# Performance work log

Measured on AMD Instinct MI355X. Metric: run time of the kernel, lower is better.

## Reference

```python
import jax, jax.numpy as jnp
import numpy as np

N_NODES = 100000
N_EDGES = 1280000
IN_DIM = 64
HID = 64
OUT_DIM = 2
N_GRAPHS = 1000
BN_EPS = 1e-5


def setup_inputs() -> dict:
    key = jax.random.key(0)
    ks = jax.random.split(key, 16)
    x = jax.random.normal(ks[0], (N_NODES, IN_DIM), dtype=jnp.float32)
    edge_index = jax.random.randint(ks[1], (2, N_EDGES), 0, N_NODES, dtype=jnp.int64)
    batch = jnp.sort(jax.random.randint(ks[2], (N_NODES,), 0, N_GRAPHS, dtype=jnp.int64))
    # He-init linear weights (stored as [in, out] so forward is x @ W)
    def he(k, fan_in, fan_out):
        return jax.random.normal(k, (fan_in, fan_out), dtype=jnp.float32) * np.sqrt(2.0 / fan_in)
    return {
        "x": x,
        "edge_index": edge_index,
        "batch": batch,
        "bn_in_g": jnp.ones((IN_DIM,), jnp.float32),
        "bn_in_b": jnp.zeros((IN_DIM,), jnp.float32),
        "W1": he(ks[3], IN_DIM, HID), "b1": jnp.zeros((HID,), jnp.float32),
        "g1": jnp.ones((HID,), jnp.float32), "be1": jnp.zeros((HID,), jnp.float32),
        "W2": he(ks[4], HID, HID), "b2": jnp.zeros((HID,), jnp.float32),
        "g2": jnp.ones((HID,), jnp.float32), "be2": jnp.zeros((HID,), jnp.float32),
        "Wout": he(ks[5], HID, OUT_DIM), "bout": jnp.zeros((OUT_DIM,), jnp.float32),
    }


def _batchnorm(x, g, b):
    # training-mode BN over the node dimension (biased variance, as torch uses for normalization)
    m = jnp.mean(x, axis=0)
    v = jnp.mean(jnp.square(x - m), axis=0)
    return (x - m) * jax.lax.rsqrt(v + BN_EPS) * g + b


def _gcn_norm(edge_index, n):
    # PyG GCNConv normalization with added self-loops:
    # norm_e = deg[src]^-1/2 * deg[dst]^-1/2, deg computed on A + I over targets.
    row = jnp.concatenate([edge_index[0], jnp.arange(n, dtype=edge_index.dtype)])
    col = jnp.concatenate([edge_index[1], jnp.arange(n, dtype=edge_index.dtype)])
    deg = jax.ops.segment_sum(jnp.ones_like(col, dtype=jnp.float32), col, num_segments=n)
    dinv = jnp.where(deg > 0, jax.lax.rsqrt(deg), 0.0)
    norm = dinv[row] * dinv[col]
    return row, col, norm


def _gcn_conv(x, W, b, row, col, norm, n):
    h = x @ W                                   # [N, out]
    msg = h[row] * norm[:, None]                # gather over edges (incl. self-loops)
    agg = jax.ops.segment_sum(msg, col, num_segments=n)
    return agg + b


def reference(x, edge_index, batch, bn_in_g, bn_in_b, W1, b1, g1, be1, W2, b2, g2, be2, Wout, bout):
    n = x.shape[0]
    row, col, norm = _gcn_norm(edge_index, n)
    h = _batchnorm(x, bn_in_g, bn_in_b)         # input BN (dropout = identity in eval)
    h = _gcn_conv(h, W1, b1, row, col, norm, n)
    h = _batchnorm(jax.nn.relu(h), g1, be1)
    h = _gcn_conv(h, W2, b2, row, col, norm, n)
    h = _batchnorm(jax.nn.relu(h), g2, be2)
    # global mean pool per graph
    sums = jax.ops.segment_sum(h, batch, num_segments=N_GRAPHS)
    cnts = jax.ops.segment_sum(jnp.ones((n,), h.dtype), batch, num_segments=N_GRAPHS)
    pooled = sums / jnp.maximum(cnts, 1.0)[:, None]
    return pooled @ Wout + bout                 # [N_GRAPHS, OUT_DIM]
```

## Files before the change

kernel.cpp:

```cpp
#include <hip/hip_runtime.h>
#include <math.h>

#define N_NODES 100000
#define N_EDGES 1280000
#define DIM 64
#define N_GRAPHS 1000
#define BN_EPS 1e-5f
#define NB 392
#define P1B 256
#define P1E 5000
#define SB 400
#define WIN 128
#define NWIN (N_EDGES / WIN)
#define GU 8
#define NSLOT 32

__device__ __forceinline__ unsigned int bf16_rtn2(float a, float b) {
    unsigned int ua = __float_as_uint(a);
    unsigned int ub = __float_as_uint(b);
    ua = (ua + 0x7FFFu + ((ua >> 16) & 1u)) >> 16;
    ub = (ub + 0x7FFFu + ((ub >> 16) & 1u)) >> 16;
    return ua | (ub << 16);
}
__device__ __forceinline__ unsigned short bf16r(float a) {
    unsigned int u = __float_as_uint(a);
    return (unsigned short)((u + 0x7FFFu + ((u >> 16) & 1u)) >> 16);
}
__device__ __forceinline__ float bfup(unsigned short u) {
    return __uint_as_float(((unsigned int)u) << 16);
}

__global__ __launch_bounds__(256) void k_p1hist(const int* __restrict__ ei,
                                                const int* __restrict__ batch,
                                                const float* __restrict__ X,
                                                int* __restrict__ bh,
                                                int* __restrict__ start,
                                                float* __restrict__ gsum,
                                                float* __restrict__ gsumsq) {
    int t = threadIdx.x;
    if (blockIdx.x < P1B) {
        __shared__ int hist[NB];
        for (int b = t; b < NB; b += 256) hist[b] = 0;
        __syncthreads();
        int e0 = blockIdx.x * P1E;
        #pragma unroll 4
        for (int e = e0 + t; e < e0 + P1E; e += 256)
            atomicAdd(&hist[ei[N_EDGES + e] >> 8], 1);
        __syncthreads();
        for (int b = t; b < NB; b += 256) bh[b * P1B + blockIdx.x] = hist[b];
    } else if (blockIdx.x < P1B + SB) {
        int grp = blockIdx.x - P1B;
        int j = t & 63, rg = t >> 6;
        int base = grp * 250;
        float s = 0.f, s2 = 0.f;
        for (int i = base + rg; i < base + 250; i += 4) {
            float v = X[i * DIM + j];
            s += v; s2 += v * v;
        }
        __shared__ float ls[256], ls2[256];
        ls[t] = s; ls2[t] = s2;
        __syncthreads();
        if (t < 64) {
            int slot = (grp & (NSLOT - 1)) * DIM;
            s  = ls[j]  + ls[64 + j]  + ls[128 + j]  + ls[192 + j];
            s2 = ls2[j] + ls2[64 + j] + ls2[128 + j] + ls2[192 + j];
            atomicAdd(&gsum[slot + j], s);
            atomicAdd(&gsumsq[slot + j], s2);
        }
    } else {
        int i = (blockIdx.x - P1B - SB) * 256 + t;
        if (i < N_NODES) {
            int cur = batch[i];
            if (i == 0) { for (int q = 0; q <= cur; q++) start[q] = 0; }
            else {
                int prev = batch[i - 1];
                for (int q = prev + 1; q <= cur; q++) start[q] = i;
            }
            if (i == N_NODES - 1)
                for (int q = cur + 1; q <= N_GRAPHS; q++) start[q] = N_NODES;
        }
    }
}

__global__ void k_scan1(const int* __restrict__ bh, int* __restrict__ iscan,
                        int* __restrict__ bsum) {
    __shared__ int ls[256];
    int i = blockIdx.x * 256 + threadIdx.x;
    int v = bh[i];
    ls[threadIdx.x] = v;
    __syncthreads();
    for (int off = 1; off < 256; off <<= 1) {
        int tv = (threadIdx.x >= off) ? ls[threadIdx.x - off] : 0;
        __syncthreads();
        ls[threadIdx.x] += tv;
        __syncthreads();
    }
    iscan[i] = ls[threadIdx.x];
    if (threadIdx.x == 255) bsum[blockIdx.x] = ls[255];
}

__global__ void k_scan2(const int* __restrict__ bsum, int* __restrict__ boff) {
    __shared__ int ls[512];
    int t = threadIdx.x;
    int v0 = (t < NB) ? bsum[t] : 0;
    ls[t] = v0;
    __syncthreads();
    for (int off = 1; off < 512; off <<= 1) {
        int v = (t >= off) ? ls[t - off] : 0;
        __syncthreads();
        ls[t] += v;
        __syncthreads();
    }
    if (t < NB) boff[t] = ls[t] - v0;
}

__global__ __launch_bounds__(256) void k_p1scat(const int* __restrict__ ei,
                                                const int* __restrict__ bh,
                                                const int* __restrict__ iscan,
                                                const int* __restrict__ boff,
                                                int2* __restrict__ tmp) {
    __shared__ int cur[NB];
    int blk = blockIdx.x;
    for (int b = threadIdx.x; b < NB; b += 256) {
        int i = b * P1B + blk;
        cur[b] = boff[b] + iscan[i] - bh[i];
    }
    __syncthreads();
    int e0 = blk * P1E;
    for (int e = e0 + threadIdx.x; e < e0 + P1E; e += 256) {
        int r = ei[e], c = ei[N_EDGES + e];
        int pos = atomicAdd(&cur[c >> 8], 1);
        tmp[pos] = make_int2(r, c);
    }
}

__global__ __launch_bounds__(256) void k_p2a(const int2* __restrict__ tmp,
                                             const int* __restrict__ bh,
                                             const int* __restrict__ iscan,
                                             const int* __restrict__ boff,
                                             int* __restrict__ rowstart,
                                             float* __restrict__ dinv,
                                             int* __restrict__ winnode) {
    int b = blockIdx.x, t = threadIdx.x;
    int bstart = boff[b] + iscan[b * 256] - bh[b * 256];
    int bend = (b == NB - 1) ? N_EDGES
                             : (boff[b + 1] + iscan[(b + 1) * 256] - bh[(b + 1) * 256]);
    __shared__ int cnt[256], scn[256];
    cnt[t] = 0;
    __syncthreads();
    for (int e = bstart + t; e < bend; e += 256)
        atomicAdd(&cnt[tmp[e].y & 255], 1);
    __syncthreads();
    scn[t] = cnt[t];
    __syncthreads();
    for (int off = 1; off < 256; off <<= 1) {
        int v = (t >= off) ? scn[t - off] : 0;
        __syncthreads();
        scn[t] += v;
        __syncthreads();
    }
    int node = b * 256 + t;
    int rs = bstart + scn[t] - cnt[t];
    if (node <= N_NODES) rowstart[node] = rs;
    if (node < N_NODES) {
        int deg = cnt[t];
        dinv[node] = 1.0f / sqrtf((float)(deg + 1));
        int re = rs + deg;
        for (int w = (rs + WIN - 1) / WIN; w * WIN < re; ++w) winnode[w] = node;
    }
}

__global__ __launch_bounds__(256) void k_p2b(const int2* __restrict__ tmp,
                                             const int* __restrict__ bh,
                                             const int* __restrict__ iscan,
                                             const int* __restrict__ boff,
                                             const int* __restrict__ rowstart,
                                             int* __restrict__ csr) {
    int b = blockIdx.x, t = threadIdx.x;
    int bstart = boff[b] + iscan[b * 256] - bh[b * 256];
    int bend = (b == NB - 1) ? N_EDGES
                             : (boff[b + 1] + iscan[(b + 1) * 256] - bh[(b + 1) * 256]);
    __shared__ int curs[256];
    int node = b * 256 + t;
    curs[t] = (node < N_NODES) ? rowstart[node] : 0;
    __syncthreads();
    for (int e = bstart + t; e < bend; e += 256) {
        int2 rec = tmp[e];
        int pos = atomicAdd(&curs[rec.y & 255], 1);
        csr[pos] = rec.x;
    }
}

__global__ void k_bnfold(float* __restrict__ gsum, float* __restrict__ gsumsq,
                         const float* __restrict__ g, const float* __restrict__ b,
                         const float* __restrict__ W,
                         float* __restrict__ scale, float* __restrict__ cshift) {
    int j = threadIdx.x;
    float ms = 0.f, m2 = 0.f;
    for (int k = 0; k < NSLOT; k++) {
        ms += gsum[k * DIM + j];   gsum[k * DIM + j] = 0.f;
        m2 += gsumsq[k * DIM + j]; gsumsq[k * DIM + j] = 0.f;
    }
    float mean = ms * (1.0f / N_NODES);
    float var  = m2 * (1.0f / N_NODES) - mean * mean;
    float inv  = 1.0f / sqrtf(var + BN_EPS);
    float sc   = g[j] * inv;
    scale[j] = sc;
    __shared__ float shl[64];
    shl[j] = b[j] - mean * sc;
    __syncthreads();
    float s = 0.f;
    for (int k = 0; k < DIM; k++) s += shl[k] * W[k * DIM + j];
    cshift[j] = s;
}

__global__ void k_bnfinal(const float* __restrict__ gsum, const float* __restrict__ gsumsq,
                          const float* __restrict__ g, const float* __restrict__ b,
                          float* __restrict__ scale, float* __restrict__ shift) {
    int j = threadIdx.x;
    float ms = 0.f, m2 = 0.f;
    for (int k = 0; k < NSLOT; k++) { ms += gsum[k * DIM + j]; m2 += gsumsq[k * DIM + j]; }
    float mean = ms * (1.0f / N_NODES);
    float var  = m2 * (1.0f / N_NODES) - mean * mean;
    float inv  = 1.0f / sqrtf(var + BN_EPS);
    float sc   = g[j] * inv;
    scale[j] = sc;
    shift[j] = b[j] - mean * sc;
}

__global__ __launch_bounds__(256) void k_gemm_f32(const float* __restrict__ X,
                                                  const float* __restrict__ W,
                                                  const float* __restrict__ scale,
                                                  const float* __restrict__ cshift,
                                                  const float* __restrict__ dinv,
                                                  unsigned short* __restrict__ T) {
    __shared__ float Wl[64 * 64];
    __shared__ float Al[64 * 65];
    for (int t = threadIdx.x; t < 4096; t += 256) Wl[t] = W[t] * scale[t >> 6];
    int row0 = blockIdx.x * 64;
    for (int t = threadIdx.x; t < 4096; t += 256) {
        int r = t >> 6, k = t & 63;
        int i = row0 + r;
        Al[r * 65 + k] = (i < N_NODES) ? X[(size_t)i * DIM + k] : 0.f;
    }
    __syncthreads();
    int r = threadIdx.x & 63;
    int q = threadIdx.x >> 6;
    float acc[16];
    #pragma unroll
    for (int jj = 0; jj < 16; jj++) acc[jj] = cshift[q * 16 + jj];
    #pragma unroll 4
    for (int k = 0; k < 64; k++) {
        float a = Al[r * 65 + k];
        const float4* wv = (const float4*)&Wl[k * 64 + q * 16];
        float4 w0 = wv[0], w1 = wv[1], w2 = wv[2], w3 = wv[3];
        acc[0]  += a * w0.x; acc[1]  += a * w0.y; acc[2]  += a * w0.z; acc[3]  += a * w0.w;
        acc[4]  += a * w1.x; acc[5]  += a * w1.y; acc[6]  += a * w1.z; acc[7]  += a * w1.w;
        acc[8]  += a * w2.x; acc[9]  += a * w2.y; acc[10] += a * w2.z; acc[11] += a * w2.w;
        acc[12] += a * w3.x; acc[13] += a * w3.y; acc[14] += a * w3.z; acc[15] += a * w3.w;
    }
    int i = row0 + r;
    if (i < N_NODES) {
        float dv = dinv[i];
        unsigned int pk[8];
        #pragma unroll
        for (int jj = 0; jj < 8; jj++)
            pk[jj] = bf16_rtn2(acc[2 * jj] * dv, acc[2 * jj + 1] * dv);
        uint4* outv = (uint4*)&T[(size_t)i * DIM + q * 16];
        outv[0] = make_uint4(pk[0], pk[1], pk[2], pk[3]);
        outv[1] = make_uint4(pk[4], pk[5], pk[6], pk[7]);
    }
}

__global__ __launch_bounds__(256) void k_gemm_b16(const unsigned short* __restrict__ X,
                                                  const float* __restrict__ W,
                                                  const float* __restrict__ scale,
                                                  const float* __restrict__ cshift,
                                                  const float* __restrict__ dinv,
                                                  unsigned short* __restrict__ T) {
    __shared__ float Wl[64 * 64];
    __shared__ float Al[64 * 65];
    for (int t = threadIdx.x; t < 4096; t += 256) Wl[t] = W[t] * scale[t >> 6];
    int row0 = blockIdx.x * 64;
    for (int t = threadIdx.x; t < 4096; t += 256) {
        int r = t >> 6, k = t & 63;
        int i = row0 + r;
        Al[r * 65 + k] = (i < N_NODES) ? bfup(X[(size_t)i * DIM + k]) : 0.f;
    }
    __syncthreads();
    int r = threadIdx.x & 63;
    int q = threadIdx.x >> 6;
    float acc[16];
    #pragma unroll
    for (int jj = 0; jj < 16; jj++) acc[jj] = cshift[q * 16 + jj];
    #pragma unroll 4
    for (int k = 0; k < 64; k++) {
        float a = Al[r * 65 + k];
        const float4* wv = (const float4*)&Wl[k * 64 + q * 16];
        float4 w0 = wv[0], w1 = wv[1], w2 = wv[2], w3 = wv[3];
        acc[0]  += a * w0.x; acc[1]  += a * w0.y; acc[2]  += a * w0.z; acc[3]  += a * w0.w;
        acc[4]  += a * w1.x; acc[5]  += a * w1.y; acc[6]  += a * w1.z; acc[7]  += a * w1.w;
        acc[8]  += a * w2.x; acc[9]  += a * w2.y; acc[10] += a * w2.z; acc[11] += a * w2.w;
        acc[12] += a * w3.x; acc[13] += a * w3.y; acc[14] += a * w3.z; acc[15] += a * w3.w;
    }
    int i = row0 + r;
    if (i < N_NODES) {
        float dv = dinv[i];
        unsigned int pk[8];
        #pragma unroll
        for (int jj = 0; jj < 8; jj++)
            pk[jj] = bf16_rtn2(acc[2 * jj] * dv, acc[2 * jj + 1] * dv);
        uint4* outv = (uint4*)&T[(size_t)i * DIM + q * 16];
        outv[0] = make_uint4(pk[0], pk[1], pk[2], pk[3]);
        outv[1] = make_uint4(pk[4], pk[5], pk[6], pk[7]);
    }
}

__global__ __launch_bounds__(256) void k_zstrad(const int* __restrict__ rowstart,
                                                const int* __restrict__ winnode,
                                                float* __restrict__ C) {
    int lane = threadIdx.x & 63;
    int w = blockIdx.x * 4 + (threadIdx.x >> 6);
    int n = winnode[w];
    if (rowstart[n] < w * WIN)
        C[(size_t)n * DIM + lane] = 0.f;
}

__global__ __launch_bounds__(256) void k_gather1(const unsigned short* __restrict__ T,
                                                 const float* __restrict__ dinv,
                                                 const int* __restrict__ rowstart,
                                                 const int* __restrict__ winnode,
                                                 const int* __restrict__ csr,
                                                 const float* __restrict__ bias,
                                                 float* __restrict__ C,
                                                 unsigned short* __restrict__ H,
                                                 float* __restrict__ gsum,
                                                 float* __restrict__ gsumsq) {
    int lane = threadIdx.x & 63;
    int w = blockIdx.x * 4 + (threadIdx.x >> 6);
    float bb = bias[lane];
    float s = 0.f, s2 = 0.f;
    int e = w * WIN;
    const int eend = e + WIN;
    int i  = __builtin_amdgcn_readfirstlane(winnode[w]);
    int re = __builtin_amdgcn_readfirstlane(rowstart[i + 1]);
    bool part = __builtin_amdgcn_readfirstlane(rowstart[i]) < e;
    float acc = 0.f;
    for (; e < eend; e += GU) {
        int src[GU];
        int eu = __builtin_amdgcn_readfirstlane(e);
        #pragma unroll
        for (int u = 0; u < GU; u++) src[u] = csr[eu + u];
        float tv[GU];
        #pragma unroll
        for (int u = 0; u < GU; u++) tv[u] = bfup(T[(size_t)src[u] * DIM + lane]);
        #pragma unroll
        for (int u = 0; u < GU; u++) {
            while (e + u == re) {
                if (part) { atomicAdd(&C[(size_t)i * DIM + lane], acc); part = false; }
                else {
                    float di = dinv[i];
                    float h = fmaxf((acc + bfup(T[(size_t)i * DIM + lane])) * di + bb, 0.f);
                    H[(size_t)i * DIM + lane] = bf16r(h);
                    s += h; s2 += h * h;
                }
                acc = 0.f; ++i;
                re = __builtin_amdgcn_readfirstlane(rowstart[i + 1]);
            }
            acc += tv[u];
        }
    }
    if (part || re > eend) atomicAdd(&C[(size_t)i * DIM + lane], acc);
    else {
        float di = dinv[i];
        float h = fmaxf((acc + bfup(T[(size_t)i * DIM + lane])) * di + bb, 0.f);
        H[(size_t)i * DIM + lane] = bf16r(h);
        s += h; s2 += h * h;
    }
    __shared__ float ls[256], ls2[256];
    ls[threadIdx.x] = s; ls2[threadIdx.x] = s2;
    __syncthreads();
    if (threadIdx.x < 64) {
        int j = threadIdx.x;
        int slot = (blockIdx.x & (NSLOT - 1)) * DIM;
        atomicAdd(&gsum[slot + j],   ls[j] + ls[64 + j] + ls[128 + j] + ls[192 + j]);
        atomicAdd(&gsumsq[slot + j], ls2[j] + ls2[64 + j] + ls2[128 + j] + ls2[192 + j]);
    }
}

__global__ __launch_bounds__(256) void k_gather2(const unsigned short* __restrict__ T,
                                                 const float* __restrict__ dinv,
                                                 const int* __restrict__ rowstart,
                                                 const int* __restrict__ winnode,
                                                 const int* __restrict__ csr,
                                                 const float* __restrict__ bias,
                                                 const int* __restrict__ batch,
                                                 float* __restrict__ C,
                                                 float* __restrict__ pool,
                                                 float* __restrict__ gsum,
                                                 float* __restrict__ gsumsq) {
    int lane = threadIdx.x & 63;
    int w = blockIdx.x * 4 + (threadIdx.x >> 6);
    float bb = bias[lane];
    float s = 0.f, s2 = 0.f, ps = 0.f;
    int cur_g = -1;
    int e = w * WIN;
    const int eend = e + WIN;
    int i  = __builtin_amdgcn_readfirstlane(winnode[w]);
    int re = __builtin_amdgcn_readfirstlane(rowstart[i + 1]);
    bool part = __builtin_amdgcn_readfirstlane(rowstart[i]) < e;
    float acc = 0.f;
    for (; e < eend; e += GU) {
        int src[GU];
        int eu = __builtin_amdgcn_readfirstlane(e);
        #pragma unroll
        for (int u = 0; u < GU; u++) src[u] = csr[eu + u];
        float tv[GU];
        #pragma unroll
        for (int u = 0; u < GU; u++) tv[u] = bfup(T[(size_t)src[u] * DIM + lane]);
        #pragma unroll
        for (int u = 0; u < GU; u++) {
            while (e + u == re) {
                if (part) { atomicAdd(&C[(size_t)i * DIM + lane], acc); part = false; }
                else {
                    float di = dinv[i];
                    float h = fmaxf((acc + bfup(T[(size_t)i * DIM + lane])) * di + bb, 0.f);
                    s += h; s2 += h * h;
                    int g = batch[i];
                    if (g != cur_g) {
                        if (cur_g >= 0) atomicAdd(&pool[(size_t)cur_g * DIM + lane], ps);
                        ps = 0.f; cur_g = g;
                    }
                    ps += h;
                }
                acc = 0.f; ++i;
                re = __builtin_amdgcn_readfirstlane(rowstart[i + 1]);
            }
            acc += tv[u];
        }
    }
    if (part || re > eend) atomicAdd(&C[(size_t)i * DIM + lane], acc);
    else {
        float di = dinv[i];
        float h = fmaxf((acc + bfup(T[(size_t)i * DIM + lane])) * di + bb, 0.f);
        s += h; s2 += h * h;
        int g = batch[i];
        if (g != cur_g) {
            if (cur_g >= 0) atomicAdd(&pool[(size_t)cur_g * DIM + lane], ps);
            ps = 0.f; cur_g = g;
        }
        ps += h;
    }
    if (cur_g >= 0) atomicAdd(&pool[(size_t)cur_g * DIM + lane], ps);
    __shared__ float ls[256], ls2[256];
    ls[threadIdx.x] = s; ls2[threadIdx.x] = s2;
    __syncthreads();
    if (threadIdx.x < 64) {
        int j = threadIdx.x;
        int slot = (blockIdx.x & (NSLOT - 1)) * DIM;
        atomicAdd(&gsum[slot + j],   ls[j] + ls[64 + j] + ls[128 + j] + ls[192 + j]);
        atomicAdd(&gsumsq[slot + j], ls2[j] + ls2[64 + j] + ls2[128 + j] + ls2[192 + j]);
    }
}

__global__ __launch_bounds__(256) void k_strad1(const float* __restrict__ C,
                                                const unsigned short* __restrict__ T,
                                                const float* __restrict__ dinv,
                                                const int* __restrict__ rowstart,
                                                const int* __restrict__ winnode,
                                                const float* __restrict__ bias,
                                                unsigned short* __restrict__ H,
                                                float* __restrict__ gsum,
                                                float* __restrict__ gsumsq) {
    int lane = threadIdx.x & 63;
    int wv = threadIdx.x >> 6;
    float bb = bias[lane];
    float s = 0.f, s2 = 0.f;
    __shared__ int anyw;
    if (threadIdx.x == 0) anyw = 0;
    __syncthreads();
    if (blockIdx.x < NWIN / 4) {
        int w = blockIdx.x * 4 + wv;
        int n = winnode[w];
        int rs = rowstart[n];
        if (w == rs / WIN + 1) {
            float di = dinv[n];
            float h = fmaxf((C[(size_t)n * DIM + lane]
                             + bfup(T[(size_t)n * DIM + lane])) * di + bb, 0.f);
            H[(size_t)n * DIM + lane] = bf16r(h);
            s += h; s2 += h * h;
            anyw = 1;
        }
    } else {
        int base = (blockIdx.x - NWIN / 4) * 256 + wv * 64;
        int nb = base + lane;
        int d0 = 0;
        if (nb < N_NODES)
            d0 = (rowstart[nb + 1] == rowstart[nb]) && ((rowstart[nb] & (WIN - 1)) == 0);
        unsigned long long m = __ballot(d0);
        while (m) {
            int b = __builtin_ctzll(m);
            m &= m - 1;
            int n = base + b;
            float di = dinv[n];
            float h = fmaxf(bfup(T[(size_t)n * DIM + lane]) * di + bb, 0.f);
            H[(size_t)n * DIM + lane] = bf16r(h);
            s += h; s2 += h * h;
            anyw = 1;
        }
    }
    __shared__ float ls[256], ls2[256];
    ls[threadIdx.x] = s; ls2[threadIdx.x] = s2;
    __syncthreads();
    if (anyw && threadIdx.x < 64) {
        int j = threadIdx.x;
        int slot = (blockIdx.x & (NSLOT - 1)) * DIM;
        atomicAdd(&gsum[slot + j],   ls[j] + ls[64 + j] + ls[128 + j] + ls[192 + j]);
        atomicAdd(&gsumsq[slot + j], ls2[j] + ls2[64 + j] + ls2[128 + j] + ls2[192 + j]);
    }
}

__global__ __launch_bounds__(256) void k_strad2(const float* __restrict__ C,
                                                const unsigned short* __restrict__ T,
                                                const float* __restrict__ dinv,
                                                const int* __restrict__ rowstart,
                                                const int* __restrict__ winnode,
                                                const float* __restrict__ bias,
                                                const int* __restrict__ batch,
                                                float* __restrict__ pool,
                                                float* __restrict__ gsum,
                                                float* __restrict__ gsumsq) {
    int lane = threadIdx.x & 63;
    int wv = threadIdx.x >> 6;
    float bb = bias[lane];
    float s = 0.f, s2 = 0.f;
    __shared__ int anyw;
    if (threadIdx.x == 0) anyw = 0;
    __syncthreads();
    if (blockIdx.x < NWIN / 4) {
        int w = blockIdx.x * 4 + wv;
        int n = winnode[w];
        int rs = rowstart[n];
        if (w == rs / WIN + 1) {
            float di = dinv[n];
            float h = fmaxf((C[(size_t)n * DIM + lane]
                             + bfup(T[(size_t)n * DIM + lane])) * di + bb, 0.f);
            s += h; s2 += h * h;
            atomicAdd(&pool[(size_t)batch[n] * DIM + lane], h);
            anyw = 1;
        }
    } else {
        int base = (blockIdx.x - NWIN / 4) * 256 + wv * 64;
        int nb = base + lane;
        int d0 = 0;
        if (nb < N_NODES)
            d0 = (rowstart[nb + 1] == rowstart[nb]) && ((rowstart[nb] & (WIN - 1)) == 0);
        unsigned long long m = __ballot(d0);
        while (m) {
            int b = __builtin_ctzll(m);
            m &= m - 1;
            int n = base + b;
            float di = dinv[n];
            float h = fmaxf(bfup(T[(size_t)n * DIM + lane]) * di + bb, 0.f);
            s += h; s2 += h * h;
            atomicAdd(&pool[(size_t)batch[n] * DIM + lane], h);
            anyw = 1;
        }
    }
    __shared__ float ls[256], ls2[256];
    ls[threadIdx.x] = s; ls2[threadIdx.x] = s2;
    __syncthreads();
    if (anyw && threadIdx.x < 64) {
        int j = threadIdx.x;
        int slot = (blockIdx.x & (NSLOT - 1)) * DIM;
        atomicAdd(&gsum[slot + j],   ls[j] + ls[64 + j] + ls[128 + j] + ls[192 + j]);
        atomicAdd(&gsumsq[slot + j], ls2[j] + ls2[64 + j] + ls2[128 + j] + ls2[192 + j]);
    }
}

__global__ void k_final(const float* __restrict__ pool, const int* __restrict__ start,
                        const float* __restrict__ scale, const float* __restrict__ shift,
                        const float* __restrict__ Wout, const float* __restrict__ bout,
                        float* __restrict__ out) {
    int g = blockIdx.x;
    int l = threadIdx.x;
    float c = fmaxf((float)(start[g + 1] - start[g]), 1.f);
    float p = (pool[g * DIM + l] / c) * scale[l] + shift[l];
    float a0 = p * Wout[l * 2 + 0];
    float a1 = p * Wout[l * 2 + 1];
    #pragma unroll
    for (int off = 32; off; off >>= 1) {
        a0 += __shfl_down(a0, off, 64);
        a1 += __shfl_down(a1, off, 64);
    }
    if (l == 0) {
        out[g * 2 + 0] = a0 + bout[0];
        out[g * 2 + 1] = a1 + bout[1];
    }
}

extern "C" void kernel_launch(void* const* d_in, const int* in_sizes, int n_in,
                              void* d_out, int out_size, void* d_ws, size_t ws_size,
                              hipStream_t stream) {
    (void)in_sizes; (void)n_in; (void)out_size; (void)ws_size;
    const float* x       = (const float*)d_in[0];
    const int*   ei      = (const int*)d_in[1];
    const int*   batch   = (const int*)d_in[2];
    const float* bn_in_g = (const float*)d_in[3];
    const float* bn_in_b = (const float*)d_in[4];
    const float* W1      = (const float*)d_in[5];
    const float* b1      = (const float*)d_in[6];
    const float* g1      = (const float*)d_in[7];
    const float* be1     = (const float*)d_in[8];
    const float* W2      = (const float*)d_in[9];
    const float* b2      = (const float*)d_in[10];
    const float* g2      = (const float*)d_in[11];
    const float* be2     = (const float*)d_in[12];
    const float* Wout    = (const float*)d_in[13];
    const float* bout    = (const float*)d_in[14];
    float* out = (float*)d_out;

    char* p = (char*)d_ws;
    float* C = (float*)p;                   p += (size_t)N_NODES * DIM * 4;
    unsigned short* H = (unsigned short*)p; p += (size_t)N_NODES * DIM * 2;
    unsigned short* T = (unsigned short*)p; p += (size_t)N_NODES * DIM * 2;
    int* csr = (int*)p;                     p += (size_t)N_EDGES * 4;
    float* dinv = (float*)p;                p += N_NODES * 4;
    int* bh = (int*)p;                      p += NB * P1B * 4;
    int* iscan = (int*)p;                   p += NB * P1B * 4;
    int* rowstart = (int*)p;                p += (N_NODES + 2) * 4;
    int* winnode = (int*)p;                 p += NWIN * 4;
    int* bsum = (int*)p;                    p += NB * 4;
    int* boff = (int*)p;                    p += NB * 4;
    int* start = (int*)p;                   p += (N_GRAPHS + 2) * 4;
    float* gsum = (float*)p;                p += NSLOT * DIM * 4;
    float* gsumsq = (float*)p;              p += NSLOT * DIM * 4;
    float* scale = (float*)p;               p += DIM * 4;
    float* shift = (float*)p;               p += DIM * 4;
    float* cshift = (float*)p;              p += DIM * 4;
    float* pool = (float*)p;                p += (size_t)N_GRAPHS * DIM * 4;
    int2* tmp = (int2*)H;

    hipMemsetAsync(gsum, 0, 2 * NSLOT * DIM * sizeof(float), stream);
    hipMemsetAsync(pool, 0, (size_t)N_GRAPHS * DIM * sizeof(float), stream);
    k_p1hist<<<P1B + SB + 392, 256, 0, stream>>>(ei, batch, x, bh, start, gsum, gsumsq);
    k_scan1<<<NB, 256, 0, stream>>>(bh, iscan, bsum);
    k_scan2<<<1, 512, 0, stream>>>(bsum, boff);
    k_p1scat<<<P1B, 256, 0, stream>>>(ei, bh, iscan, boff, tmp);
    k_p2a<<<NB, 256, 0, stream>>>(tmp, bh, iscan, boff, rowstart, dinv, winnode);
    k_p2b<<<NB, 256, 0, stream>>>(tmp, bh, iscan, boff, rowstart, csr);

    k_bnfold<<<1, 64, 0, stream>>>(gsum, gsumsq, bn_in_g, bn_in_b, W1, scale, cshift);
    k_gemm_f32<<<(N_NODES + 63) / 64, 256, 0, stream>>>(x, W1, scale, cshift, dinv, T);
    k_zstrad<<<NWIN / 4, 256, 0, stream>>>(rowstart, winnode, C);
    k_gather1<<<NWIN / 4, 256, 0, stream>>>(T, dinv, rowstart, winnode, csr, b1,
                                            C, H, gsum, gsumsq);
    k_strad1<<<NWIN / 4 + 392, 256, 0, stream>>>(C, T, dinv, rowstart, winnode, b1,
                                                 H, gsum, gsumsq);

    k_bnfold<<<1, 64, 0, stream>>>(gsum, gsumsq, g1, be1, W2, scale, cshift);
    k_gemm_b16<<<(N_NODES + 63) / 64, 256, 0, stream>>>(H, W2, scale, cshift, dinv, T);
    k_zstrad<<<NWIN / 4, 256, 0, stream>>>(rowstart, winnode, C);
    k_gather2<<<NWIN / 4, 256, 0, stream>>>(T, dinv, rowstart, winnode, csr, b2,
                                            batch, C, pool, gsum, gsumsq);
    k_strad2<<<NWIN / 4 + 392, 256, 0, stream>>>(C, T, dinv, rowstart, winnode, b2,
                                                 batch, pool, gsum, gsumsq);

    k_bnfinal<<<1, 64, 0, stream>>>(gsum, gsumsq, g2, be2, scale, shift);
    k_final<<<N_GRAPHS, 64, 0, stream>>>(pool, start, scale, shift, Wout, bout, out);
}
```

Measured before the change: 335.1 us.

## Pack edge records into one int and fold straddle-row zeroing into existing kernels

The intermediate edge buffer now stores each edge as a single 32-bit word (source shifted left by 8, low 8 bits of destination) instead of an int2, halving scatter and read traffic in the CSR build. The two separate zeroing kernels for the accumulator rows of nodes spanning edge windows are removed. Zeroing now happens once in the CSR kernel, and the layer-1 straddle kernel resets C after reading it so layer 2 starts from zero. This saves two launches and some traffic, but relies on source ids fitting in 24 bits and on the reset in the straddle kernel covering exactly the rows layer 2 accumulates into.

```diff
diff --git a/kernel.cpp b/kernel.cpp
--- a/kernel.cpp
+++ b/kernel.cpp
@@ -118,7 +118,7 @@
                                                 const int* __restrict__ bh,
                                                 const int* __restrict__ iscan,
                                                 const int* __restrict__ boff,
-                                                int2* __restrict__ tmp) {
+                                                int* __restrict__ tmp) {
     __shared__ int cur[NB];
     int blk = blockIdx.x;
     for (int b = threadIdx.x; b < NB; b += 256) {
@@ -130,17 +130,18 @@
     for (int e = e0 + threadIdx.x; e < e0 + P1E; e += 256) {
         int r = ei[e], c = ei[N_EDGES + e];
         int pos = atomicAdd(&cur[c >> 8], 1);
-        tmp[pos] = make_int2(r, c);
-    }
-}
-
-__global__ __launch_bounds__(256) void k_p2a(const int2* __restrict__ tmp,
+        tmp[pos] = (r << 8) | (c & 255);
+    }
+}
+
+__global__ __launch_bounds__(256) void k_p2a(const int* __restrict__ tmp,
                                              const int* __restrict__ bh,
                                              const int* __restrict__ iscan,
                                              const int* __restrict__ boff,
                                              int* __restrict__ rowstart,
                                              float* __restrict__ dinv,
-                                             int* __restrict__ winnode) {
+                                             int* __restrict__ winnode,
+                                             float* __restrict__ C) {
     int b = blockIdx.x, t = threadIdx.x;
     int bstart = boff[b] + iscan[b * 256] - bh[b * 256];
     int bend = (b == NB - 1) ? N_EDGES
@@ -149,7 +150,7 @@
     cnt[t] = 0;
     __syncthreads();
     for (int e = bstart + t; e < bend; e += 256)
-        atomicAdd(&cnt[tmp[e].y & 255], 1);
+        atomicAdd(&cnt[tmp[e] & 255], 1);
     __syncthreads();
     scn[t] = cnt[t];
     __syncthreads();
@@ -160,17 +161,27 @@
         __syncthreads();
     }
     int node = b * 256 + t;
-    int rs = bstart + scn[t] - cnt[t];
+    int deg = cnt[t];
+    int rs = bstart + scn[t] - deg;
+    bool span = false;
     if (node <= N_NODES) rowstart[node] = rs;
     if (node < N_NODES) {
-        int deg = cnt[t];
         dinv[node] = 1.0f / sqrtf((float)(deg + 1));
         int re = rs + deg;
         for (int w = (rs + WIN - 1) / WIN; w * WIN < re; ++w) winnode[w] = node;
-    }
-}
-
-__global__ __launch_bounds__(256) void k_p2b(const int2* __restrict__ tmp,
+        span = (deg > 0) && (rs / WIN != (re - 1) / WIN);
+    }
+    int lane = t & 63;
+    int wbase = b * 256 + (t & ~63);
+    unsigned long long m = __ballot(span);
+    while (m) {
+        int bit = __builtin_ctzll(m);
+        m &= m - 1;
+        C[(size_t)(wbase + bit) * DIM + lane] = 0.f;
+    }
+}
+
+__global__ __launch_bounds__(256) void k_p2b(const int* __restrict__ tmp,
                                              const int* __restrict__ bh,
                                              const int* __restrict__ iscan,
                                              const int* __restrict__ boff,
@@ -185,9 +196,9 @@
     curs[t] = (node < N_NODES) ? rowstart[node] : 0;
     __syncthreads();
     for (int e = bstart + t; e < bend; e += 256) {
-        int2 rec = tmp[e];
-        int pos = atomicAdd(&curs[rec.y & 255], 1);
-        csr[pos] = rec.x;
+        int rec = tmp[e];
+        int pos = atomicAdd(&curs[rec & 255], 1);
+        csr[pos] = (int)((unsigned)rec >> 8);
     }
 }
 
@@ -314,16 +325,6 @@
         outv[0] = make_uint4(pk[0], pk[1], pk[2], pk[3]);
         outv[1] = make_uint4(pk[4], pk[5], pk[6], pk[7]);
     }
-}
-
-__global__ __launch_bounds__(256) void k_zstrad(const int* __restrict__ rowstart,
-                                                const int* __restrict__ winnode,
-                                                float* __restrict__ C) {
-    int lane = threadIdx.x & 63;
-    int w = blockIdx.x * 4 + (threadIdx.x >> 6);
-    int n = winnode[w];
-    if (rowstart[n] < w * WIN)
-        C[(size_t)n * DIM + lane] = 0.f;
 }
 
 __global__ __launch_bounds__(256) void k_gather1(const unsigned short* __restrict__ T,
@@ -463,7 +464,7 @@
     }
 }
 
-__global__ __launch_bounds__(256) void k_strad1(const float* __restrict__ C,
+__global__ __launch_bounds__(256) void k_strad1(float* __restrict__ C,
                                                 const unsigned short* __restrict__ T,
                                                 const float* __restrict__ dinv,
                                                 const int* __restrict__ rowstart,
@@ -485,8 +486,9 @@
         int rs = rowstart[n];
         if (w == rs / WIN + 1) {
             float di = dinv[n];
-            float h = fmaxf((C[(size_t)n * DIM + lane]
-                             + bfup(T[(size_t)n * DIM + lane])) * di + bb, 0.f);
+            float c = C[(size_t)n * DIM + lane];
+            C[(size_t)n * DIM + lane] = 0.f;
+            float h = fmaxf((c + bfup(T[(size_t)n * DIM + lane])) * di + bb, 0.f);
             H[(size_t)n * DIM + lane] = bf16r(h);
             s += h; s2 += h * h;
             anyw = 1;
@@ -639,7 +641,7 @@
     float* shift = (float*)p;               p += DIM * 4;
     float* cshift = (float*)p;              p += DIM * 4;
     float* pool = (float*)p;                p += (size_t)N_GRAPHS * DIM * 4;
-    int2* tmp = (int2*)H;
+    int* tmp = (int*)H;
 
     hipMemsetAsync(gsum, 0, 2 * NSLOT * DIM * sizeof(float), stream);
     hipMemsetAsync(pool, 0, (size_t)N_GRAPHS * DIM * sizeof(float), stream);
@@ -647,12 +649,11 @@
     k_scan1<<<NB, 256, 0, stream>>>(bh, iscan, bsum);
     k_scan2<<<1, 512, 0, stream>>>(bsum, boff);
     k_p1scat<<<P1B, 256, 0, stream>>>(ei, bh, iscan, boff, tmp);
-    k_p2a<<<NB, 256, 0, stream>>>(tmp, bh, iscan, boff, rowstart, dinv, winnode);
+    k_p2a<<<NB, 256, 0, stream>>>(tmp, bh, iscan, boff, rowstart, dinv, winnode, C);
     k_p2b<<<NB, 256, 0, stream>>>(tmp, bh, iscan, boff, rowstart, csr);
 
     k_bnfold<<<1, 64, 0, stream>>>(gsum, gsumsq, bn_in_g, bn_in_b, W1, scale, cshift);
     k_gemm_f32<<<(N_NODES + 63) / 64, 256, 0, stream>>>(x, W1, scale, cshift, dinv, T);
-    k_zstrad<<<NWIN / 4, 256, 0, stream>>>(rowstart, winnode, C);
     k_gather1<<<NWIN / 4, 256, 0, stream>>>(T, dinv, rowstart, winnode, csr, b1,
                                             C, H, gsum, gsumsq);
     k_strad1<<<NWIN / 4 + 392, 256, 0, stream>>>(C, T, dinv, rowstart, winnode, b1,
@@ -660,7 +661,6 @@
 
     k_bnfold<<<1, 64, 0, stream>>>(gsum, gsumsq, g1, be1, W2, scale, cshift);
     k_gemm_b16<<<(N_NODES + 63) / 64, 256, 0, stream>>>(H, W2, scale, cshift, dinv, T);
-    k_zstrad<<<NWIN / 4, 256, 0, stream>>>(rowstart, winnode, C);
     k_gather2<<<NWIN / 4, 256, 0, stream>>>(T, dinv, rowstart, winnode, csr, b2,
                                             batch, C, pool, gsum, gsumsq);
     k_strad2<<<NWIN / 4 + 392, 256, 0, stream>>>(C, T, dinv, rowstart, winnode, b2,
```

New measurement: 330.4 us. No clear change (-1.4%).
